# Optimization experiments

Hardware: AMD Instinct MI355X
Metric: run time of the kernel (lower is better)

Reference implementation:

```python
import jax, jax.numpy as jnp
import numpy as np

B, F, C, O, M = 128, 4096, 32, 32, 9  # batch, num_fields, in_ch, out_ch, num_coeffs (moves incl. self)


def setup_inputs() -> dict:
    key = jax.random.key(0)
    k1, k2, k3, k4 = jax.random.split(key, 4)
    x = jax.random.normal(k1, (B, F, C), dtype=jnp.float32)
    # mask[m, f] = index of the source field feeding target field f via move m
    mask = jax.random.randint(k2, (M, F), 0, F, dtype=jnp.int32)
    init_std = 1.0 / (3.0 * np.sqrt(C * O))  # matches TruncatedNormal stddev in build()
    conv_coeffs = jax.random.normal(k3, (M, C, O), dtype=jnp.float32) * init_std
    # biases are zero-initialized in the original; use small random values so the
    # bias-add path is exercised numerically
    biases = jax.random.normal(k4, (F, O), dtype=jnp.float32) * 0.01
    return {"x": x, "mask": mask, "conv_coeffs": conv_coeffs, "biases": biases}


def reference(x, mask, conv_coeffs, biases):
    # ch_convolve_by_moves: gather source fields per move, per-move matmul, per-field bias.
    # gathered[b, m, f, c] = x[b, mask[m, f], c]
    gathered = jnp.take(x, mask, axis=1)              # [B, M, F, C]
    out = jnp.einsum('bmfc,mco->bfo', gathered, conv_coeffs)  # sum over moves and in-channels
    return out + biases                               # per-field bias broadcast over batch
```

## Files before the change

### kernel.cpp

```cpp
#include <hip/hip_runtime.h>


#define B_ 128
#define F_ 4096
#define C_ 32
#define O_ 32
#define M_ 9
#define T_ 18
#define FPB 2
#define TF 16
#define TB 32
#define LROW (TB * C_ + 8)

typedef _Float16 halfx4 __attribute__((ext_vector_type(4)));
typedef _Float16 halfx8 __attribute__((ext_vector_type(8)));
typedef float floatx16 __attribute__((ext_vector_type(16)));

__global__ __launch_bounds__(256) void pass1_transpose(
    const float* __restrict__ x, const float* __restrict__ coeffs,
    _Float16* __restrict__ xh, _Float16* __restrict__ wf)
{
    __shared__ _Float16 tile[TF * LROW];
    const int tid  = threadIdx.x;
    const int f0   = blockIdx.x * TF;
    const int b0   = blockIdx.y * TB;
    const int tsub = tid & 127;
    const int grp  = tid >> 7;

    {
        const int f_l = tsub >> 3;
        const int c4  = (tsub & 7) * 4;
#pragma unroll
        for (int it = 0; it < TB / 2; ++it) {
            int b_l = it * 2 + grp;
            float4 v = *reinterpret_cast<const float4*>(
                x + ((size_t)(b0 + b_l) * F_ + f0 + f_l) * C_ + c4);
            halfx4 hv;
            hv[0] = (_Float16)v.x; hv[1] = (_Float16)v.y;
            hv[2] = (_Float16)v.z; hv[3] = (_Float16)v.w;
            *reinterpret_cast<halfx4*>(&tile[f_l * LROW + b_l * C_ + c4]) = hv;
        }
    }
    __syncthreads();

    {
        const int b_l = tsub >> 2;
        const int c8  = (tsub & 3) * 8;
#pragma unroll
        for (int it = 0; it < TF / 2; ++it) {
            int f_l = it * 2 + grp;
            halfx8 v = *reinterpret_cast<const halfx8*>(&tile[f_l * LROW + b_l * C_ + c8]);
            *reinterpret_cast<halfx8*>(
                xh + ((size_t)(f0 + f_l) * B_ + b0 + b_l) * C_ + c8) = v;
        }
    }

    if (blockIdx.x == 0 && blockIdx.y == 0) {
        for (int id = threadIdx.x; id < T_ * 64; id += 256) {
            int t  = id >> 6;
            int L  = id & 63;
            int m  = t >> 1;
            int cb = 16 * (t & 1) + 8 * (L >> 5);
            int o  = L & 31;
            halfx8 w;
#pragma unroll
            for (int j = 0; j < 8; ++j)
                w[j] = (_Float16)coeffs[(m * C_ + cb + j) * O_ + o];
            *reinterpret_cast<halfx8*>(wf + id * 8) = w;
        }
    }
}

__global__ __launch_bounds__(256, 4) void pass2_gemm(
    const _Float16* __restrict__ xh, const _Float16* __restrict__ wf,
    const int* __restrict__ mask, const float* __restrict__ biases,
    float* __restrict__ out)
{
    __shared__ _Float16 sw[T_ * 64 * 8];
    const int tid = threadIdx.x;
#pragma unroll
    for (int i = tid; i < T_ * 64; i += 256)
        *reinterpret_cast<halfx8*>(&sw[i * 8]) = reinterpret_cast<const halfx8*>(wf)[i];
    __syncthreads();

    const int lane  = tid & 63;
    const int wave  = tid >> 6;
    const int r32   = lane & 31;
    const int h     = lane >> 5;
    const int bbase = wave * 32;
    const int f0    = blockIdx.x * FPB;

    const _Float16* xbase = xh + (size_t)(bbase + r32) * C_ + 8 * h;

    for (int fi = 0; fi < FPB; ++fi) {
        const int f = f0 + fi;
        halfx8 a[T_];
#pragma unroll
        for (int m = 0; m < M_; ++m) {
            const _Float16* rp = xbase + (size_t)mask[m * F_ + f] * (B_ * C_);
            a[2 * m]     = *reinterpret_cast<const halfx8*>(rp);
            a[2 * m + 1] = *reinterpret_cast<const halfx8*>(rp + 16);
        }
        floatx16 acc;
#pragma unroll
        for (int i = 0; i < 16; ++i) acc[i] = 0.0f;
#pragma unroll
        for (int t = 0; t < T_; ++t) {
            halfx8 bwt = *reinterpret_cast<const halfx8*>(&sw[(t * 64 + lane) * 8]);
            acc = __builtin_amdgcn_mfma_f32_32x32x16_f16(a[t], bwt, acc, 0, 0, 0);
        }
        float bias = biases[f * O_ + r32];
#pragma unroll
        for (int r = 0; r < 16; ++r) {
            int orow = (r & 3) + 8 * (r >> 2) + 4 * h;
            out[((size_t)(bbase + orow) * F_ + f) * O_ + r32] = acc[r] + bias;
        }
    }
}

__global__ __launch_bounds__(256) void fallback_kernel(
    const float* __restrict__ x, const int* __restrict__ mask,
    const float* __restrict__ coeffs, const float* __restrict__ biases,
    float* __restrict__ out)
{
    int gid = blockIdx.x * 256 + threadIdx.x;
    int o = gid & (O_ - 1);
    int f = (gid >> 5) & (F_ - 1);
    int b = gid >> 17;
    float acc = biases[f * O_ + o];
    for (int m = 0; m < M_; ++m) {
        int s = mask[m * F_ + f];
        const float* xr = x + ((size_t)b * F_ + s) * C_;
        const float* wr = coeffs + (m * C_) * O_ + o;
#pragma unroll
        for (int c = 0; c < C_; ++c)
            acc += xr[c] * wr[c * O_];
    }
    out[gid] = acc;
}

extern "C" void kernel_launch(void* const* d_in, const int* in_sizes, int n_in,
                              void* d_out, int out_size, void* d_ws, size_t ws_size,
                              hipStream_t stream) {
    const float* x      = (const float*)d_in[0];
    const int*   mask   = (const int*)d_in[1];
    const float* coeffs = (const float*)d_in[2];
    const float* biases = (const float*)d_in[3];
    float* out = (float*)d_out;

    const size_t xh_elems = (size_t)B_ * F_ * C_;
    const size_t need = xh_elems * sizeof(_Float16) + (size_t)T_ * 64 * 8 * sizeof(_Float16);

    if (ws_size >= need) {
        _Float16* xh = (_Float16*)d_ws;
        _Float16* wf = xh + xh_elems;
        dim3 g1(F_ / TF, B_ / TB);
        pass1_transpose<<<g1, 256, 0, stream>>>(x, coeffs, xh, wf);
        pass2_gemm<<<F_ / FPB, 256, 0, stream>>>(xh, wf, mask, biases, out);
    } else {
        fallback_kernel<<<(B_ * F_ * O_) / 256, 256, 0, stream>>>(x, mask, coeffs, biases, out);
    }
}
```

Baseline: 164.0 us.

## Re-layout fp16 workspace into batch-slices and remap GEMM tiles to 16 batches × 2 fields

The intermediate fp16 copy of x is reorganized into 8 batch slices of 16, stored field-major as [bs][f][16][C], so each gathered source field yields a contiguous 1 KB chunk. The GEMM kernel now gives each wave 2 fields × 16 batches as the 32 MFMA rows, with one launch covering 8 fields per batch slice. The aim is better locality for the gathered rows and more parallel blocks. Nontemporal loads of x and stores of out are added to cut cache pollution, at the cost of smaller per-gather contiguity across batches and more blocks.

```diff
diff --git a/kernel.cpp b/kernel.cpp
--- a/kernel.cpp
+++ b/kernel.cpp
@@ -7,56 +7,55 @@
 #define O_ 32
 #define M_ 9
 #define T_ 18
-#define FPB 2
-#define TF 16
-#define TB 32
-#define LROW (TB * C_ + 8)
+#define TF1 32
+#define LROW1 528
 
 typedef _Float16 halfx4 __attribute__((ext_vector_type(4)));
 typedef _Float16 halfx8 __attribute__((ext_vector_type(8)));
+typedef float floatx4 __attribute__((ext_vector_type(4)));
 typedef float floatx16 __attribute__((ext_vector_type(16)));
 
 __global__ __launch_bounds__(256) void pass1_transpose(
     const float* __restrict__ x, const float* __restrict__ coeffs,
     _Float16* __restrict__ xh, _Float16* __restrict__ wf)
 {
-    __shared__ _Float16 tile[TF * LROW];
-    const int tid  = threadIdx.x;
-    const int f0   = blockIdx.x * TF;
-    const int b0   = blockIdx.y * TB;
-    const int tsub = tid & 127;
-    const int grp  = tid >> 7;
+    __shared__ _Float16 tile[TF1 * LROW1];
+    const int blk = blockIdx.x;
+    const int bs  = blk & 7;
+    const int f0  = (blk >> 3) * TF1;
+    const int tid = threadIdx.x;
 
     {
-        const int f_l = tsub >> 3;
-        const int c4  = (tsub & 7) * 4;
+        const int f_l = tid >> 3;
+        const int c4  = (tid & 7) * 4;
+        const float* src = x + ((size_t)f0 + f_l) * C_ + c4;
 #pragma unroll
-        for (int it = 0; it < TB / 2; ++it) {
-            int b_l = it * 2 + grp;
-            float4 v = *reinterpret_cast<const float4*>(
-                x + ((size_t)(b0 + b_l) * F_ + f0 + f_l) * C_ + c4);
+        for (int bp = 0; bp < 16; ++bp) {
+            const floatx4* p = reinterpret_cast<const floatx4*>(
+                src + (size_t)(bs * 16 + bp) * (F_ * C_));
+            floatx4 v = __builtin_nontemporal_load(p);
             halfx4 hv;
-            hv[0] = (_Float16)v.x; hv[1] = (_Float16)v.y;
-            hv[2] = (_Float16)v.z; hv[3] = (_Float16)v.w;
-            *reinterpret_cast<halfx4*>(&tile[f_l * LROW + b_l * C_ + c4]) = hv;
+            hv[0] = (_Float16)v[0]; hv[1] = (_Float16)v[1];
+            hv[2] = (_Float16)v[2]; hv[3] = (_Float16)v[3];
+            *reinterpret_cast<halfx4*>(&tile[f_l * LROW1 + bp * C_ + c4]) = hv;
         }
     }
     __syncthreads();
 
     {
-        const int b_l = tsub >> 2;
-        const int c8  = (tsub & 3) * 8;
+        const int wv   = tid >> 6;
+        const int lane = tid & 63;
 #pragma unroll
-        for (int it = 0; it < TF / 2; ++it) {
-            int f_l = it * 2 + grp;
-            halfx8 v = *reinterpret_cast<const halfx8*>(&tile[f_l * LROW + b_l * C_ + c8]);
+        for (int it = 0; it < TF1 / 4; ++it) {
+            int f_l = it * 4 + wv;
+            halfx8 v = *reinterpret_cast<const halfx8*>(&tile[f_l * LROW1 + lane * 8]);
             *reinterpret_cast<halfx8*>(
-                xh + ((size_t)(f0 + f_l) * B_ + b0 + b_l) * C_ + c8) = v;
+                xh + ((size_t)bs * F_ + f0 + f_l) * (16 * C_) + lane * 8) = v;
         }
     }
 
-    if (blockIdx.x == 0 && blockIdx.y == 0) {
-        for (int id = threadIdx.x; id < T_ * 64; id += 256) {
+    if (blk == 0) {
+        for (int id = tid; id < T_ * 64; id += 256) {
             int t  = id >> 6;
             int L  = id & 63;
             int m  = t >> 1;
@@ -80,41 +79,56 @@
     const int tid = threadIdx.x;
 #pragma unroll
     for (int i = tid; i < T_ * 64; i += 256)
-        *reinterpret_cast<halfx8*>(&sw[i * 8]) = reinterpret_cast<const halfx8*>(wf)[i];
+        reinterpret_cast<halfx8*>(sw)[i] = reinterpret_cast<const halfx8*>(wf)[i];
     __syncthreads();
 
-    const int lane  = tid & 63;
-    const int wave  = tid >> 6;
-    const int r32   = lane & 31;
-    const int h     = lane >> 5;
-    const int bbase = wave * 32;
-    const int f0    = blockIdx.x * FPB;
+    const int blk  = blockIdx.x;
+    const int bs   = blk & 7;
+    const int fg   = blk >> 3;
+    const int wave = tid >> 6;
+    const int lane = tid & 63;
+    const int h    = lane >> 5;
+    const int row  = lane & 31;
+    const int fi   = row >> 4;
+    const int bp   = row & 15;
+    const int ocol = lane & 31;
 
-    const _Float16* xbase = xh + (size_t)(bbase + r32) * C_ + 8 * h;
+    const int fa = fg * 8 + 2 * wave;
+    const int f  = fa + fi;
 
-    for (int fi = 0; fi < FPB; ++fi) {
-        const int f = f0 + fi;
-        halfx8 a[T_];
+    const _Float16* xb = xh + (size_t)bs * F_ * (16 * C_) + bp * C_ + 8 * h;
+
+    int sidx[M_];
 #pragma unroll
-        for (int m = 0; m < M_; ++m) {
-            const _Float16* rp = xbase + (size_t)mask[m * F_ + f] * (B_ * C_);
-            a[2 * m]     = *reinterpret_cast<const halfx8*>(rp);
-            a[2 * m + 1] = *reinterpret_cast<const halfx8*>(rp + 16);
-        }
-        floatx16 acc;
+    for (int m = 0; m < M_; ++m) sidx[m] = mask[m * F_ + f];
+
+    halfx8 a[T_];
 #pragma unroll
-        for (int i = 0; i < 16; ++i) acc[i] = 0.0f;
+    for (int m = 0; m < M_; ++m) {
+        const _Float16* rp = xb + (size_t)sidx[m] * (16 * C_);
+        a[2 * m]     = *reinterpret_cast<const halfx8*>(rp);
+        a[2 * m + 1] = *reinterpret_cast<const halfx8*>(rp + 16);
+    }
+
+    floatx16 acc;
 #pragma unroll
-        for (int t = 0; t < T_; ++t) {
-            halfx8 bwt = *reinterpret_cast<const halfx8*>(&sw[(t * 64 + lane) * 8]);
-            acc = __builtin_amdgcn_mfma_f32_32x32x16_f16(a[t], bwt, acc, 0, 0, 0);
-        }
-        float bias = biases[f * O_ + r32];
+    for (int i = 0; i < 16; ++i) acc[i] = 0.0f;
 #pragma unroll
-        for (int r = 0; r < 16; ++r) {
-            int orow = (r & 3) + 8 * (r >> 2) + 4 * h;
-            out[((size_t)(bbase + orow) * F_ + f) * O_ + r32] = acc[r] + bias;
-        }
+    for (int t = 0; t < T_; ++t) {
+        halfx8 bwt = *reinterpret_cast<const halfx8*>(&sw[(t * 64 + lane) * 8]);
+        acc = __builtin_amdgcn_mfma_f32_32x32x16_f16(a[t], bwt, acc, 0, 0, 0);
+    }
+
+    float bias_a = biases[(size_t)fa * O_ + ocol];
+    float bias_b = biases[(size_t)(fa + 1) * O_ + ocol];
+#pragma unroll
+    for (int r = 0; r < 16; ++r) {
+        int orow = (r & 3) + 8 * (r >> 2) + 4 * h;
+        int ofi  = orow >> 4;
+        int b    = bs * 16 + (orow & 15);
+        float v  = acc[r] + (ofi ? bias_b : bias_a);
+        __builtin_nontemporal_store(
+            v, &out[((size_t)b * F_ + fa + ofi) * O_ + ocol]);
     }
 }
 
@@ -154,9 +168,8 @@
     if (ws_size >= need) {
         _Float16* xh = (_Float16*)d_ws;
         _Float16* wf = xh + xh_elems;
-        dim3 g1(F_ / TF, B_ / TB);
-        pass1_transpose<<<g1, 256, 0, stream>>>(x, coeffs, xh, wf);
-        pass2_gemm<<<F_ / FPB, 256, 0, stream>>>(xh, wf, mask, biases, out);
+        pass1_transpose<<<8 * (F_ / TF1), 256, 0, stream>>>(x, coeffs, xh, wf);
+        pass2_gemm<<<8 * (F_ / 8), 256, 0, stream>>>(xh, wf, mask, biases, out);
     } else {
         fallback_kernel<<<(B_ * F_ * O_) / 256, 256, 0, stream>>>(x, mask, coeffs, biases, out);
     }
```

New measurement: 143.5 us. 1.14x faster.
